# Performance work log

Hardware: AMD Instinct MI355X
Metric: run time of the kernel (lower is better)

Reference implementation:

```python
import jax, jax.numpy as jnp
import numpy as np

T = 16384
G = 8
D_IN = 2048
D_OUT = 8192
# uneven per-expert group sizes summing exactly to T (torch.split requires this)
_GROUP_SIZES = np.array([1024, 3072, 2048, 512, 4096, 1536, 2560, 1536], dtype=np.int64)
assert _GROUP_SIZES.sum() == T


def setup_inputs() -> dict:
    key = jax.random.key(0)
    k_x, k_w = jax.random.split(key)
    hidden_states = jax.random.normal(k_x, (T, D_IN), dtype=jnp.float32)
    # kaiming_uniform_(a=sqrt(5)) on [G, out, in] -> bound = 1/sqrt(in_features)
    bound = 1.0 / np.sqrt(D_IN)
    weight = jax.random.uniform(k_w, (G, D_OUT, D_IN), dtype=jnp.float32,
                                minval=-bound, maxval=bound)
    offsets = jnp.asarray(np.cumsum(_GROUP_SIZES), dtype=jnp.int64)
    return {"hidden_states": hidden_states, "offsets": offsets, "weight": weight}


def reference(hidden_states, offsets, weight):
    # grouped GEMM: for group g, rows [offsets[g-1]:offsets[g]] @ weight[g].T
    # weight is [G, out, in]; torch transposes last two dims -> rhs [G, in, out]
    group_sizes = jnp.diff(offsets, prepend=jnp.zeros((1,), offsets.dtype)).astype(jnp.int32)
    rhs = jnp.swapaxes(weight, -1, -2)  # [G, in, out]
    return jax.lax.ragged_dot(hidden_states, rhs, group_sizes)  # [T, out]
```

## Files before the change

### kernel.cpp

```cpp
#include <hip/hip_runtime.h>
#include <stdint.h>

#define T_TOK   16384
#define D_INK   2048
#define D_OUTN  8192
#define G_NUM   8

#define BM 128
#define BN 128
#define BK 32
#define NKT (D_INK / BK)
#define MT_TILES (T_TOK / BM)
#define NT_TILES (D_OUTN / BN)
#define MCHUNK 8

typedef __attribute__((ext_vector_type(8))) short bf16x8;
typedef __attribute__((ext_vector_type(4))) float f32x4;

__device__ __forceinline__ unsigned int f2bf(float f) {
    union { float f; unsigned int u; } v; v.f = f;
    unsigned int u = v.u;
    unsigned int r = u + 0x7FFFu + ((u >> 16) & 1u);
    return r >> 16;
}

__global__ __launch_bounds__(256) void cvt_f32_bf16(const float* __restrict__ src,
                                                    unsigned short* __restrict__ dst,
                                                    long long n8) {
    long long i = (long long)blockIdx.x * blockDim.x + threadIdx.x;
    long long stride = (long long)gridDim.x * blockDim.x;
    const float4* s4 = reinterpret_cast<const float4*>(src);
    for (; i < n8; i += stride) {
        float4 x = s4[i * 2];
        float4 y = s4[i * 2 + 1];
        uint4 o;
        o.x = f2bf(x.x) | (f2bf(x.y) << 16);
        o.y = f2bf(x.z) | (f2bf(x.w) << 16);
        o.z = f2bf(y.x) | (f2bf(y.y) << 16);
        o.w = f2bf(y.z) | (f2bf(y.w) << 16);
        *reinterpret_cast<uint4*>(dst + i * 8) = o;
    }
}

__device__ __forceinline__ void gload_lds16(const unsigned short* g, void* l) {
    __builtin_amdgcn_global_load_lds(
        (const __attribute__((address_space(1))) void*)g,
        (__attribute__((address_space(3))) void*)l,
        16, 0, 0);
}

__global__ __launch_bounds__(256, 3) void grouped_gemm_bf16(
    const unsigned short* __restrict__ Abf,
    const unsigned short* __restrict__ Wbf,
    const int* __restrict__ offs_raw,
    float* __restrict__ out)
{
    __shared__ unsigned short ldsA[2][BM][BK];
    __shared__ unsigned short ldsB[2][BN][BK];

    const int tid  = threadIdx.x;
    const int wave = tid >> 6;
    const int lane = tid & 63;

    const int nwg = gridDim.x;
    const int cpx = nwg >> 3;
    const int swz = (blockIdx.x & 7) * cpx + (blockIdx.x >> 3);
    const int per_chunk = MCHUNK * NT_TILES;
    const int chunk = swz / per_chunk;
    const int rem   = swz % per_chunk;
    const int nt = rem >> 3;
    const int mt = chunk * MCHUNK + (rem & (MCHUNK - 1));

    const int row0 = mt * BM;
    const int col0 = nt * BN;

    const int ostride = (offs_raw[1] == 0) ? 2 : 1;
    int g = 0;
#pragma unroll
    for (int i = 0; i < G_NUM - 1; ++i)
        if (row0 >= offs_raw[i * ostride]) g = i + 1;

    const unsigned short* Aorig = Abf + (size_t)row0 * D_INK;
    const unsigned short* Worig = Wbf + ((size_t)g * D_OUTN + col0) * D_INK;

    const int srow = lane >> 2;
    const int sk   = (lane & 3) * 8;

    const int fr = lane & 15;
    const int fk = (lane >> 4) * 8;
    const int wm = (wave >> 1) * 64;
    const int wn = (wave & 1) * 64;

    f32x4 acc[4][4] = {};

    auto stage = [&](int buf, int kt) {
        const int kbase = kt * BK + sk;
#pragma unroll
        for (int c2 = 0; c2 < 2; ++c2) {
            const int chnk = wave * 2 + c2;
            const int r = chnk * 16 + srow;
            gload_lds16(Aorig + (size_t)r * D_INK + kbase,
                        (char*)(&ldsA[buf][0][0]) + chnk * 1024);
            gload_lds16(Worig + (size_t)r * D_INK + kbase,
                        (char*)(&ldsB[buf][0][0]) + chnk * 1024);
        }
    };

    stage(0, 0);
    int buf = 0;
    for (int kt = 0; kt < NKT; ++kt) {
        __syncthreads();
        if (kt + 1 < NKT) stage(buf ^ 1, kt + 1);

        bf16x8 a[4], b[4];
#pragma unroll
        for (int i = 0; i < 4; ++i)
            a[i] = *reinterpret_cast<const bf16x8*>(&ldsA[buf][wm + i * 16 + fr][fk]);
#pragma unroll
        for (int j = 0; j < 4; ++j)
            b[j] = *reinterpret_cast<const bf16x8*>(&ldsB[buf][wn + j * 16 + fr][fk]);
#pragma unroll
        for (int i = 0; i < 4; ++i)
#pragma unroll
            for (int j = 0; j < 4; ++j)
                acc[i][j] = __builtin_amdgcn_mfma_f32_16x16x32_bf16(a[i], b[j], acc[i][j], 0, 0, 0);
        buf ^= 1;
    }

    const int crb = (lane >> 4) * 4;
#pragma unroll
    for (int i = 0; i < 4; ++i)
#pragma unroll
        for (int j = 0; j < 4; ++j)
#pragma unroll
            for (int r = 0; r < 4; ++r) {
                const int rr = row0 + wm + i * 16 + crb + r;
                const int cc = col0 + wn + j * 16 + fr;
                out[(size_t)rr * D_OUTN + cc] = acc[i][j][r];
            }
}

__global__ __launch_bounds__(256) void naive_grouped(
    const float* __restrict__ A, const float* __restrict__ W,
    const int* __restrict__ offs_raw, float* __restrict__ out)
{
    const long long total = (long long)T_TOK * D_OUTN;
    long long idx = (long long)blockIdx.x * blockDim.x + threadIdx.x;
    const long long stride = (long long)gridDim.x * blockDim.x;
    const int ostride = (offs_raw[1] == 0) ? 2 : 1;
    for (; idx < total; idx += stride) {
        const int t = (int)(idx / D_OUTN);
        const int c = (int)(idx % D_OUTN);
        int g = 0;
        for (int i = 0; i < G_NUM - 1; ++i)
            if (t >= offs_raw[i * ostride]) g = i + 1;
        const float4* a4 = reinterpret_cast<const float4*>(A + (size_t)t * D_INK);
        const float4* w4 = reinterpret_cast<const float4*>(W + ((size_t)g * D_OUTN + c) * D_INK);
        float s = 0.f;
        for (int k = 0; k < D_INK / 4; ++k) {
            float4 av = a4[k], wv = w4[k];
            s += av.x * wv.x + av.y * wv.y + av.z * wv.z + av.w * wv.w;
        }
        out[idx] = s;
    }
}

extern "C" void kernel_launch(void* const* d_in, const int* in_sizes, int n_in,
                              void* d_out, int out_size, void* d_ws, size_t ws_size,
                              hipStream_t stream) {
    const float* hidden = (const float*)d_in[0];
    const int*   offs   = (const int*)d_in[1];
    const float* weight = (const float*)d_in[2];
    float* out = (float*)d_out;

    const size_t nA = (size_t)T_TOK * D_INK;
    const size_t nW = (size_t)G_NUM * D_OUTN * D_INK;
    const size_t need = (nA + nW) * sizeof(unsigned short);

    if (ws_size >= need) {
        unsigned short* Abf = (unsigned short*)d_ws;
        unsigned short* Wbf = Abf + nA;
        cvt_f32_bf16<<<2048, 256, 0, stream>>>(hidden, Abf, (long long)(nA / 8));
        cvt_f32_bf16<<<4096, 256, 0, stream>>>(weight, Wbf, (long long)(nW / 8));
        grouped_gemm_bf16<<<MT_TILES * NT_TILES, 256, 0, stream>>>(Abf, Wbf, offs, out);
    } else {
        naive_grouped<<<8192, 256, 0, stream>>>(hidden, weight, offs, out);
    }
}
```

Before: 879.8 us.

## Rewrite grouped GEMM as 256x256x64 tile with swizzled LDS and interleaved prefetch

Replaces the 128x128x32 four-wave kernel with a 256x256x64 tile run by eight waves (512 threads). Global-to-LDS loads are issued two k-steps ahead and interleaved between four MFMA phases, with explicit barriers, vmcnt waits and s_setprio to keep MFMA busy. The LDS layout uses an XOR swizzle to avoid bank conflicts. The aim is more data reuse per tile and better overlap of memory with compute, at the cost of more registers and LDS, lower occupancy, and fragile hand-placed synchronisation.

```diff
diff --git a/kernel.cpp b/kernel.cpp
--- a/kernel.cpp
+++ b/kernel.cpp
@@ -6,16 +6,20 @@
 #define D_OUTN  8192
 #define G_NUM   8
 
-#define BM 128
-#define BN 128
-#define BK 32
+#define BM 256
+#define BN 256
+#define BK 64
 #define NKT (D_INK / BK)
 #define MT_TILES (T_TOK / BM)
 #define NT_TILES (D_OUTN / BN)
-#define MCHUNK 8
+#define MCHUNK 4
 
 typedef __attribute__((ext_vector_type(8))) short bf16x8;
 typedef __attribute__((ext_vector_type(4))) float f32x4;
+
+#define BARRIER() do { asm volatile("" ::: "memory"); __builtin_amdgcn_s_barrier(); asm volatile("" ::: "memory"); } while (0)
+#define LGKM0()   asm volatile("s_waitcnt lgkmcnt(0)" ::: "memory")
+#define VMCNT(n)  asm volatile("s_waitcnt vmcnt(" #n ")" ::: "memory")
 
 __device__ __forceinline__ unsigned int f2bf(float f) {
     union { float f; unsigned int u; } v; v.f = f;
@@ -49,26 +53,23 @@
         16, 0, 0);
 }
 
-__global__ __launch_bounds__(256, 3) void grouped_gemm_bf16(
+__global__ __launch_bounds__(512, 2) void grouped_gemm_256(
     const unsigned short* __restrict__ Abf,
     const unsigned short* __restrict__ Wbf,
     const int* __restrict__ offs_raw,
     float* __restrict__ out)
 {
-    __shared__ unsigned short ldsA[2][BM][BK];
-    __shared__ unsigned short ldsB[2][BN][BK];
+    __shared__ unsigned short lds[2][32768];
 
     const int tid  = threadIdx.x;
     const int wave = tid >> 6;
     const int lane = tid & 63;
 
-    const int nwg = gridDim.x;
-    const int cpx = nwg >> 3;
-    const int swz = (blockIdx.x & 7) * cpx + (blockIdx.x >> 3);
+    const int swz = (blockIdx.x & 7) * (MT_TILES * NT_TILES / 8) + (blockIdx.x >> 3);
     const int per_chunk = MCHUNK * NT_TILES;
     const int chunk = swz / per_chunk;
     const int rem   = swz % per_chunk;
-    const int nt = rem >> 3;
+    const int nt = rem >> 2;
     const int mt = chunk * MCHUNK + (rem & (MCHUNK - 1));
 
     const int row0 = mt * BM;
@@ -83,53 +84,124 @@
     const unsigned short* Aorig = Abf + (size_t)row0 * D_INK;
     const unsigned short* Worig = Wbf + ((size_t)g * D_OUTN + col0) * D_INK;
 
-    const int srow = lane >> 2;
-    const int sk   = (lane & 3) * 8;
-
-    const int fr = lane & 15;
-    const int fk = (lane >> 4) * 8;
-    const int wm = (wave >> 1) * 64;
-    const int wn = (wave & 1) * 64;
-
-    f32x4 acc[4][4] = {};
-
-    auto stage = [&](int buf, int kt) {
-        const int kbase = kt * BK + sk;
-#pragma unroll
-        for (int c2 = 0; c2 < 2; ++c2) {
-            const int chnk = wave * 2 + c2;
-            const int r = chnk * 16 + srow;
-            gload_lds16(Aorig + (size_t)r * D_INK + kbase,
-                        (char*)(&ldsA[buf][0][0]) + chnk * 1024);
-            gload_lds16(Worig + (size_t)r * D_INK + kbase,
-                        (char*)(&ldsB[buf][0][0]) + chnk * 1024);
+    const int lrow = lane >> 2;
+    const int gcol_off = ((lane & 3) * 8) ^ ((lane & 32) ? 16 : 0);
+
+    const int fr  = lane & 15;
+    const int fk2 = (lane >> 4) << 4;
+    const int swz_off = fr * 64 + (fk2 ^ ((fr & 8) ? 32 : 0));
+    const int wm16 = (wave >> 2) * 8;
+    const int wn16 = (wave & 3) * 4;
+    const int wm = (wave >> 2) * 128;
+    const int wn = (wave & 3) * 64;
+
+    char* ldsc = (char*)&lds[0][0];
+
+    auto stageA = [&](int buf, int kt) {
+#pragma unroll
+        for (int i = 0; i < 4; ++i) {
+            const int s = wave * 4 + i;
+            const int sr = s >> 1, sc = s & 1;
+            const unsigned short* src = Aorig + (size_t)(sr * 16 + lrow) * D_INK
+                                        + kt * BK + sc * 32 + gcol_off;
+            gload_lds16(src, ldsc + buf * 65536 + s * 1024);
         }
     };
-
-    stage(0, 0);
-    int buf = 0;
-    for (int kt = 0; kt < NKT; ++kt) {
-        __syncthreads();
-        if (kt + 1 < NKT) stage(buf ^ 1, kt + 1);
-
-        bf16x8 a[4], b[4];
-#pragma unroll
-        for (int i = 0; i < 4; ++i)
-            a[i] = *reinterpret_cast<const bf16x8*>(&ldsA[buf][wm + i * 16 + fr][fk]);
-#pragma unroll
-        for (int j = 0; j < 4; ++j)
-            b[j] = *reinterpret_cast<const bf16x8*>(&ldsB[buf][wn + j * 16 + fr][fk]);
-#pragma unroll
-        for (int i = 0; i < 4; ++i)
-#pragma unroll
-            for (int j = 0; j < 4; ++j)
-                acc[i][j] = __builtin_amdgcn_mfma_f32_16x16x32_bf16(a[i], b[j], acc[i][j], 0, 0, 0);
-        buf ^= 1;
+    auto stageB = [&](int buf, int kt) {
+#pragma unroll
+        for (int i = 0; i < 4; ++i) {
+            const int s = wave * 4 + i;
+            const int sr = s >> 1, sc = s & 1;
+            const unsigned short* src = Worig + (size_t)(sr * 16 + lrow) * D_INK
+                                        + kt * BK + sc * 32 + gcol_off;
+            gload_lds16(src, ldsc + buf * 65536 + 32768 + s * 1024);
+        }
+    };
+    auto ldA = [&](int buf, int sr, int ks) -> bf16x8 {
+        return *reinterpret_cast<const bf16x8*>(ldsc + buf * 65536 + (sr * 2 + ks) * 1024 + swz_off);
+    };
+    auto ldB = [&](int buf, int sr, int ks) -> bf16x8 {
+        return *reinterpret_cast<const bf16x8*>(ldsc + buf * 65536 + 32768 + (sr * 2 + ks) * 1024 + swz_off);
+    };
+
+    f32x4 acc[8][4] = {};
+    bf16x8 a[4][2], b[4][2];
+
+    stageB(0, 0); stageA(0, 0);
+    stageB(1, 1); stageA(1, 1);
+    VMCNT(8);
+    BARRIER();
+
+    for (int t = 0; t < NKT; ++t) {
+        const int buf = t & 1;
+
+#pragma unroll
+        for (int i = 0; i < 4; ++i) { a[i][0] = ldA(buf, wm16 + i, 0); a[i][1] = ldA(buf, wm16 + i, 1); }
+#pragma unroll
+        for (int j = 0; j < 2; ++j) { b[j][0] = ldB(buf, wn16 + j, 0); b[j][1] = ldB(buf, wn16 + j, 1); }
+        BARRIER();
+        LGKM0();
+        __builtin_amdgcn_s_setprio(1);
+#pragma unroll
+        for (int i = 0; i < 4; ++i)
+#pragma unroll
+            for (int j = 0; j < 2; ++j) {
+                acc[i][j] = __builtin_amdgcn_mfma_f32_16x16x32_bf16(a[i][0], b[j][0], acc[i][j], 0, 0, 0);
+                acc[i][j] = __builtin_amdgcn_mfma_f32_16x16x32_bf16(a[i][1], b[j][1], acc[i][j], 0, 0, 0);
+            }
+        __builtin_amdgcn_s_setprio(0);
+        BARRIER();
+
+#pragma unroll
+        for (int j = 2; j < 4; ++j) { b[j][0] = ldB(buf, wn16 + j, 0); b[j][1] = ldB(buf, wn16 + j, 1); }
+        BARRIER();
+        LGKM0();
+        __builtin_amdgcn_s_setprio(1);
+#pragma unroll
+        for (int i = 0; i < 4; ++i)
+#pragma unroll
+            for (int j = 2; j < 4; ++j) {
+                acc[i][j] = __builtin_amdgcn_mfma_f32_16x16x32_bf16(a[i][0], b[j][0], acc[i][j], 0, 0, 0);
+                acc[i][j] = __builtin_amdgcn_mfma_f32_16x16x32_bf16(a[i][1], b[j][1], acc[i][j], 0, 0, 0);
+            }
+        __builtin_amdgcn_s_setprio(0);
+        BARRIER();
+
+#pragma unroll
+        for (int i = 0; i < 4; ++i) { a[i][0] = ldA(buf, wm16 + 4 + i, 0); a[i][1] = ldA(buf, wm16 + 4 + i, 1); }
+        if (t + 2 < NKT) stageB(buf, t + 2);
+        BARRIER();
+        LGKM0();
+        __builtin_amdgcn_s_setprio(1);
+#pragma unroll
+        for (int i = 0; i < 4; ++i)
+#pragma unroll
+            for (int j = 0; j < 2; ++j) {
+                acc[4 + i][j] = __builtin_amdgcn_mfma_f32_16x16x32_bf16(a[i][0], b[j][0], acc[4 + i][j], 0, 0, 0);
+                acc[4 + i][j] = __builtin_amdgcn_mfma_f32_16x16x32_bf16(a[i][1], b[j][1], acc[4 + i][j], 0, 0, 0);
+            }
+        __builtin_amdgcn_s_setprio(0);
+        BARRIER();
+
+        if (t + 2 < NKT) stageA(buf, t + 2);
+        BARRIER();
+        __builtin_amdgcn_s_setprio(1);
+#pragma unroll
+        for (int i = 0; i < 4; ++i)
+#pragma unroll
+            for (int j = 2; j < 4; ++j) {
+                acc[4 + i][j] = __builtin_amdgcn_mfma_f32_16x16x32_bf16(a[i][0], b[j][0], acc[4 + i][j], 0, 0, 0);
+                acc[4 + i][j] = __builtin_amdgcn_mfma_f32_16x16x32_bf16(a[i][1], b[j][1], acc[4 + i][j], 0, 0, 0);
+            }
+        __builtin_amdgcn_s_setprio(0);
+        if (t + 2 < NKT)      { VMCNT(8); }
+        else if (t + 1 < NKT) { VMCNT(0); }
+        BARRIER();
     }
 
     const int crb = (lane >> 4) * 4;
 #pragma unroll
-    for (int i = 0; i < 4; ++i)
+    for (int i = 0; i < 8; ++i)
 #pragma unroll
         for (int j = 0; j < 4; ++j)
 #pragma unroll
@@ -182,7 +254,7 @@
         unsigned short* Wbf = Abf + nA;
         cvt_f32_bf16<<<2048, 256, 0, stream>>>(hidden, Abf, (long long)(nA / 8));
         cvt_f32_bf16<<<4096, 256, 0, stream>>>(weight, Wbf, (long long)(nW / 8));
-        grouped_gemm_bf16<<<MT_TILES * NT_TILES, 256, 0, stream>>>(Abf, Wbf, offs, out);
+        grouped_gemm_256<<<MT_TILES * NT_TILES, 512, 0, stream>>>(Abf, Wbf, offs, out);
     } else {
         naive_grouped<<<8192, 256, 0, stream>>>(hidden, weight, offs, out);
     }
```

Result: faster. 794.1 us (-9.7%).
